# Kernel tuning notes

Hardware: AMD Instinct MI355X
Metric: run time of the kernel (lower is better)

## Reference

```python
import jax, jax.numpy as jnp
import numpy as np

N = 4096      # nodes
E = 131072    # edges (avg degree 32)
C = 256       # in/hidden channels
NC = 10       # classes
RATIO = 0.5
DEPTH = 2


def _build_adj(edge_index, w, n):
    # COO -> dense, duplicate edges summed (matches CSR coalescing)
    A = jnp.zeros((n, n), jnp.float32)
    return A.at[edge_index[0], edge_index[1]].add(w)


def _gcn(x, A, W, b, fill=2.0):
    # gcn_norm with improved=True: add_remaining_self_loops(fill=2.0),
    # deg from target (col) sums, sym norm; out[i] = sum_j Anorm[j,i] * (xW)[j]
    n = A.shape[0]
    idx = jnp.arange(n)
    diag = A[idx, idx]
    A = A.at[idx, idx].set(jnp.where(diag != 0, diag, fill))
    deg = A.sum(axis=0)
    dinv = jnp.where(deg > 0, jax.lax.rsqrt(deg), 0.0)
    An = dinv[:, None] * A * dinv[None, :]
    return An.T @ (x @ W) + b


def _augment(A):
    # remove_self_loops + add_self_loops(weight 1) == set diag to 1,
    # then adj @ adj, then remove self loops again
    n = A.shape[0]
    idx = jnp.arange(n)
    A = A.at[idx, idx].set(1.0)
    A2 = A @ A
    return A2.at[idx, idx].set(0.0)


def _pool(x, A, p, k):
    # TopKPooling: score = tanh(x.p / ||p||), keep top-k nodes, gate x by score
    score = jnp.tanh((x @ p) / jnp.linalg.norm(p))
    vals, perm = jax.lax.top_k(score, k)
    x2 = x[perm] * vals[:, None]
    A2 = A[perm][:, perm]   # filter_adj: keep edges with both ends selected
    return x2, A2


def reference(x, edge_index, w0, b0, w1, b1, w2, b2, p1, p2, wc, bc):
    A = _build_adj(edge_index, jnp.ones((edge_index.shape[1],), x.dtype), x.shape[0])
    x = jax.nn.relu(_gcn(x, A, w0, b0))
    k = x.shape[0]
    for (W, b, p) in ((w1, b1, p1), (w2, b2, p2)):
        A = _augment(A)
        k = int(np.ceil(RATIO * k))  # static per level (single graph)
        x, A = _pool(x, A, p, k)
        x = jax.nn.relu(_gcn(x, A, W, b))
    emb = x.mean(axis=0, keepdims=True)                      # global_mean_pool, batch all-zero
    emb = emb / jnp.maximum(jnp.linalg.norm(emb, axis=-1, keepdims=True), 1e-12)
    logits = emb @ wc.T + bc
    return emb, jax.nn.log_softmax(logits, axis=1)


def setup_inputs() -> dict:
    key = jax.random.key(0)
    ks = jax.random.split(key, 12)
    s = 1.0 / np.sqrt(C)
    return {
        'x': jax.random.normal(ks[0], (N, C), jnp.float32),
        'edge_index': jax.random.randint(ks[1], (2, E), 0, N, jnp.int64) if jax.config.jax_enable_x64 else jax.random.randint(ks[1], (2, E), 0, N, jnp.int32),
        'w0': jax.random.normal(ks[2], (C, C), jnp.float32) * s,
        'b0': jnp.zeros((C,), jnp.float32),
        'w1': jax.random.normal(ks[3], (C, C), jnp.float32) * s,
        'b1': jnp.zeros((C,), jnp.float32),
        'w2': jax.random.normal(ks[4], (C, C), jnp.float32) * s,
        'b2': jnp.zeros((C,), jnp.float32),
        'p1': jax.random.normal(ks[5], (C,), jnp.float32) * s,
        'p2': jax.random.normal(ks[6], (C,), jnp.float32) * s,
        'wc': jax.random.normal(ks[7], (NC, C), jnp.float32) * s,
        'bc': jnp.zeros((NC,), jnp.float32),
    }
```

## Files before the change

### kernel.cpp

```cpp
#include <hip/hip_runtime.h>
#include <math.h>

#define CH 256

typedef short short8 __attribute__((ext_vector_type(8)));
typedef float f32x4 __attribute__((ext_vector_type(4)));

__device__ inline ushort f2bf(float f) {
  unsigned u = __float_as_uint(f);
  unsigned r = (u + 0x7FFFu + ((u >> 16) & 1u)) >> 16;
  return (ushort)r;
}

__device__ inline void gload16(const void* g, void* l) {
  __builtin_amdgcn_global_load_lds((const __attribute__((address_space(1))) void*)g,
                                   (__attribute__((address_space(3))) void*)l, 16, 0, 0);
}


__global__ void scatter_edges(const int* __restrict__ ei, int E, int n, float* __restrict__ A) {
  int e = blockIdx.x * blockDim.x + threadIdx.x;
  if (e < E) atomicAdd(&A[(size_t)ei[e] * n + ei[E + e]], 1.0f);
}

template <int DIAGMODE>
__global__ __launch_bounds__(256) void transpose_deg(const float* __restrict__ In, int n,
                                                     ushort* __restrict__ O, float* __restrict__ deg,
                                                     int zn, size_t zoff) {
  __shared__ float t[64][65];
  int j0 = blockIdx.x * 64, i0 = blockIdx.y * 64;
  int tx = threadIdx.x & 63, ty4 = threadIdx.x >> 6;
  float s = 0.f;
#pragma unroll
  for (int r = 0; r < 64; r += 4) {
    int gi = i0 + ty4 + r, gj = j0 + tx;
    size_t idx = (size_t)gi * n + gj;
    float v = In[idx];
    for (int z = 1; z < zn; ++z) v += In[idx + (size_t)z * zoff];
    if (gi == gj) v = (DIAGMODE == 1) ? 2.0f : ((v != 0.f) ? v : 2.0f);
    t[ty4 + r][tx] = v;
    s += v;
  }
  atomicAdd(&deg[j0 + tx], s);
  __syncthreads();
#pragma unroll
  for (int r = 0; r < 64; r += 4) {
    int c = ty4 + r;
    O[(size_t)(j0 + c) * n + i0 + tx] = f2bf(t[tx][c]);
  }
}

__global__ __launch_bounds__(256) void topk_rank(const float* __restrict__ sc, int n, int k,
                                                 int* __restrict__ perm, float* __restrict__ vals) {
  extern __shared__ unsigned long long kbuf[];
  __shared__ int red[4][64];
  int tid = threadIdx.x;
  for (int i = tid; i < n; i += 256) {
    unsigned u = __float_as_uint(sc[i]);
    u = (u & 0x80000000u) ? ~u : (u | 0x80000000u);
    kbuf[i] = ((unsigned long long)u << 32) | (0xFFFFFFFFu - (unsigned)i);
  }
  __syncthreads();
  const int ti = tid & 63, tj = tid >> 6;
  const int i = blockIdx.x * 64 + ti;
  const unsigned long long ki = kbuf[i];
  int cnt = 0;
  const int q = n >> 2;
  const int jb = tj * q, je = jb + q;
#pragma unroll 4
  for (int j = jb; j < je; j += 2) {
    unsigned long long k0 = kbuf[j], k1 = kbuf[j + 1];
    cnt += (k0 > ki) + (k1 > ki);
  }
  red[tj][ti] = cnt;
  __syncthreads();
  if (tid < 64) {
    int r = red[0][ti] + red[1][ti] + red[2][ti] + red[3][ti];
    if (r < k) { perm[r] = i; vals[r] = sc[i]; }
  }
}

__global__ __launch_bounds__(256) void gather_fused(const float* __restrict__ Asrc, int zn, size_t zoff,
                                                    const ushort* __restrict__ At,
                                                    const int* __restrict__ perm, int n,
                                                    ushort* __restrict__ Arow, ushort* __restrict__ Brow,
                                                    const float* __restrict__ xin,
                                                    const float* __restrict__ vals, float* __restrict__ xo,
                                                    int nbcvt, int nbbf) {
  int bx = blockIdx.x;
  int m = blockIdx.y;
  int src = perm[m];
  if (bx < nbcvt) {
    int k4 = (bx * 256 + threadIdx.x) * 4;
    float4 v = *(const float4*)&Asrc[(size_t)src * n + k4];
    for (int z = 1; z < zn; ++z) {
      float4 u = *(const float4*)&Asrc[(size_t)z * zoff + (size_t)src * n + k4];
      v.x += u.x; v.y += u.y; v.z += u.z; v.w += u.w;
    }
    if (src >= k4 && src < k4 + 4) ((float*)&v)[src - k4] = 1.0f;
    ushort4 o;
    o.x = f2bf(v.x); o.y = f2bf(v.y); o.z = f2bf(v.z); o.w = f2bf(v.w);
    *(ushort4*)&Arow[(size_t)m * n + k4] = o;
  } else if (bx < nbcvt + nbbf) {
    int k8 = ((bx - nbcvt) * 256 + threadIdx.x) * 8;
    uint4 v = *(const uint4*)&At[(size_t)src * n + k8];
    if (src >= k8 && src < k8 + 8) ((ushort*)&v)[src - k8] = 0x3F80;
    *(uint4*)&Brow[(size_t)m * n + k8] = v;
  } else {
    xo[(size_t)m * CH + threadIdx.x] = xin[(size_t)src * CH + threadIdx.x] * vals[m];
  }
}


template <int BN>
__device__ inline void stage_tile(const ushort* ag, const ushort* bg, int ktOff,
                                  char* asb, char* bsb, int K) {
#pragma unroll
  for (int i = 0; i < 4; ++i)
    gload16(ag + (size_t)i * 32 * K + ktOff, asb + i * 4096);
#pragma unroll
  for (int i = 0; i < BN / 32; ++i)
    gload16(bg + (size_t)i * 32 * K + ktOff, bsb + i * 4096);
}

template <int BN>
__device__ inline void compute_tile(const ushort (*__restrict__ As)[64],
                                    const ushort (*__restrict__ Bs)[64],
                                    int wm, int wn, int lrow, int col0, int col1,
                                    f32x4 acc[4][BN / 32]) {
#pragma unroll
  for (int ks = 0; ks < 2; ++ks) {
    const int col = ks ? col1 : col0;
    short8 af[4], bf[BN / 32];
#pragma unroll
    for (int t = 0; t < 4; ++t)
      af[t] = *(const short8*)&As[wm + t * 16 + lrow][col];
#pragma unroll
    for (int t = 0; t < BN / 32; ++t)
      bf[t] = *(const short8*)&Bs[wn + t * 16 + lrow][col];
#pragma unroll
    for (int mt = 0; mt < 4; ++mt)
#pragma unroll
      for (int nt = 0; nt < BN / 32; ++nt)
        acc[mt][nt] = __builtin_amdgcn_mfma_f32_16x16x32_bf16(af[mt], bf[nt], acc[mt][nt], 0, 0, 0);
  }
}

template <int BN>
__global__ __launch_bounds__(256) void mfma_nt(const ushort* __restrict__ Aop,
                                               const ushort* __restrict__ Bop,
                                               float* __restrict__ C, int ldc,
                                               int K, int Ks, size_t zstride) {
  constexpr int NBUF = (BN == 128) ? 2 : 3;
  constexpr int NT = BN / 32;
  __shared__ ushort As[NBUF][128][64];
  __shared__ ushort Bs[NBUF][BN][64];
  const int tid = threadIdx.x;
  const int wave = tid >> 6, lane = tid & 63;
  const int wm = (wave & 1) * 64, wn = (wave >> 1) * (BN / 2);
  const int m0 = blockIdx.x * 128, n0 = blockIdx.y * BN;
  const int k0 = blockIdx.z * Ks;
  C += (size_t)blockIdx.z * zstride;
  const int lrow = lane & 15;
  const int q = lane >> 4;
  const int rx = lane & 7;
  const int col0 = ((q)     ^ rx) * 8;
  const int col1 = ((4 + q) ^ rx) * 8;
  const int srow = wave * 8 + (lane >> 3);
  const int scol = ((lane & 7) ^ (lane >> 3)) * 8;
  const ushort* ag = Aop + (size_t)(m0 + srow) * K + k0 + scol;
  const ushort* bg = Bop + (size_t)(n0 + srow) * K + k0 + scol;
  f32x4 acc[4][NT] = {};

  const int nk = Ks >> 6;

#define STAGE(bi, idx) stage_tile<BN>(ag, bg, (idx) * 64, \
    (char*)&As[bi][0][0] + wave * 1024, (char*)&Bs[bi][0][0] + wave * 1024, K)

  if constexpr (NBUF == 2) {
    STAGE(0, 0);
    if (1 < nk) STAGE(1, 1);
    int bi = 0;
    for (int t = 0; t < nk - 1; ++t) {
      asm volatile("s_waitcnt vmcnt(8)" ::: "memory");
      __builtin_amdgcn_s_barrier();
      __builtin_amdgcn_sched_barrier(0);
      compute_tile<BN>(As[bi], Bs[bi], wm, wn, lrow, col0, col1, acc);
      __builtin_amdgcn_sched_barrier(0);
      __builtin_amdgcn_s_barrier();
      if (t + 2 < nk) STAGE(bi, t + 2);
      bi ^= 1;
    }
    asm volatile("s_waitcnt vmcnt(0)" ::: "memory");
    __builtin_amdgcn_s_barrier();
    __builtin_amdgcn_sched_barrier(0);
    compute_tile<BN>(As[bi], Bs[bi], wm, wn, lrow, col0, col1, acc);
  } else {
    STAGE(0, 0);
    if (1 < nk) STAGE(1, 1);
    if (2 < nk) STAGE(2, 2);
    int bi = 0;
    for (int t = 0; t < nk - 2; ++t) {
      asm volatile("s_waitcnt vmcnt(12)" ::: "memory");
      __builtin_amdgcn_s_barrier();
      __builtin_amdgcn_sched_barrier(0);
      compute_tile<BN>(As[bi], Bs[bi], wm, wn, lrow, col0, col1, acc);
      __builtin_amdgcn_sched_barrier(0);
      __builtin_amdgcn_s_barrier();
      if (t + 3 < nk) STAGE(bi, t + 3);
      bi = (bi + 1 < 3) ? bi + 1 : 0;
    }
    asm volatile("s_waitcnt vmcnt(6)" ::: "memory");
    __builtin_amdgcn_s_barrier();
    __builtin_amdgcn_sched_barrier(0);
    compute_tile<BN>(As[bi], Bs[bi], wm, wn, lrow, col0, col1, acc);
    bi = (bi + 1 < 3) ? bi + 1 : 0;
    asm volatile("s_waitcnt vmcnt(0)" ::: "memory");
    __builtin_amdgcn_s_barrier();
    __builtin_amdgcn_sched_barrier(0);
    compute_tile<BN>(As[bi], Bs[bi], wm, wn, lrow, col0, col1, acc);
  }
#undef STAGE

  const int crow = (lane >> 4) * 4, ccol = lane & 15;
#pragma unroll
  for (int mt = 0; mt < 4; ++mt)
#pragma unroll
    for (int nt = 0; nt < NT; ++nt) {
      int gm = m0 + wm + mt * 16 + crow;
      int gn = n0 + wn + nt * 16 + ccol;
#pragma unroll
      for (int r = 0; r < 4; ++r)
        C[(size_t)(gm + r) * ldc + gn] = acc[mt][nt][r];
    }
}

__global__ void agg_epilogue(const float* __restrict__ Cred, size_t zstride, int zn,
                             float* __restrict__ deg,
                             const float* __restrict__ bias, float* __restrict__ xo,
                             const float* __restrict__ p, float* __restrict__ sc,
                             float* __restrict__ mclr) {
  int idx = blockIdx.x * 256 + threadIdx.x;
  int c4 = idx & 63;
  int m = idx >> 6;
  float d = deg[m];
  float s = (d > 0.f) ? 1.0f / sqrtf(d) : 0.f;
  if ((threadIdx.x & 63) == 0) deg[m] = 0.f;
  if (mclr && blockIdx.x == 0) mclr[threadIdx.x] = 0.f;
  float4 v = ((const float4*)Cred)[idx];
  for (int z = 1; z < zn; ++z) {
    float4 u = ((const float4*)(Cred + (size_t)z * zstride))[idx];
    v.x += u.x; v.y += u.y; v.z += u.z; v.w += u.w;
  }
  float4 b = ((const float4*)bias)[c4];
  v.x = fmaxf(fmaf(v.x, s, b.x), 0.f);
  v.y = fmaxf(fmaf(v.y, s, b.y), 0.f);
  v.z = fmaxf(fmaf(v.z, s, b.z), 0.f);
  v.w = fmaxf(fmaf(v.w, s, b.w), 0.f);
  ((float4*)xo)[idx] = v;
  if (p) {
    float4 pv = ((const float4*)p)[c4];
    float dot = v.x * pv.x + v.y * pv.y + v.z * pv.z + v.w * pv.w;
    float pn  = pv.x * pv.x + pv.y * pv.y + pv.z * pv.z + pv.w * pv.w;
    for (int off = 32; off; off >>= 1) {
      dot += __shfl_down(dot, off);
      pn  += __shfl_down(pn, off);
    }
    if ((threadIdx.x & 63) == 0) sc[m] = tanhf(dot / sqrtf(pn));
  }
}

__global__ __launch_bounds__(256) void xw_gemm(const float* __restrict__ Am,
                                               const float* __restrict__ Bm,
                                               ushort* __restrict__ Gt,
                                               int M, const float* __restrict__ deg) {
  __shared__ float As[16][64];
  __shared__ float Bs[16][64];
  const int tid = threadIdx.x;
  const int m0 = blockIdx.x * 64, n0 = blockIdx.y * 64;
  float acc[4][4] = {{0.f}};
  const int tm = tid & 15, tn = tid >> 4;

  for (int kt = 0; kt < CH; kt += 16) {
    __syncthreads();
    {
      int mm = tid >> 2, kq = (tid & 3) * 4;
      float4 v = *(const float4*)(Am + (size_t)(m0 + mm) * CH + kt + kq);
      As[kq + 0][mm] = v.x; As[kq + 1][mm] = v.y; As[kq + 2][mm] = v.z; As[kq + 3][mm] = v.w;
    }
#pragma unroll
    for (int r = 0; r < 4; ++r) {
      int idx = tid + r * 256;
      int kk = idx >> 6, nn = idx & 63;
      Bs[kk][nn] = Bm[(size_t)(kt + kk) * CH + (n0 + nn)];
    }
    __syncthreads();
#pragma unroll
    for (int kk = 0; kk < 16; ++kk) {
      float4 a = *(const float4*)&As[kk][tm * 4];
      float4 b = *(const float4*)&Bs[kk][tn * 4];
      acc[0][0] = fmaf(a.x, b.x, acc[0][0]);
      acc[0][1] = fmaf(a.x, b.y, acc[0][1]);
      acc[0][2] = fmaf(a.x, b.z, acc[0][2]);
      acc[0][3] = fmaf(a.x, b.w, acc[0][3]);
      acc[1][0] = fmaf(a.y, b.x, acc[1][0]);
      acc[1][1] = fmaf(a.y, b.y, acc[1][1]);
      acc[1][2] = fmaf(a.y, b.z, acc[1][2]);
      acc[1][3] = fmaf(a.y, b.w, acc[1][3]);
      acc[2][0] = fmaf(a.z, b.x, acc[2][0]);
      acc[2][1] = fmaf(a.z, b.y, acc[2][1]);
      acc[2][2] = fmaf(a.z, b.z, acc[2][2]);
      acc[2][3] = fmaf(a.z, b.w, acc[2][3]);
      acc[3][0] = fmaf(a.w, b.x, acc[3][0]);
      acc[3][1] = fmaf(a.w, b.y, acc[3][1]);
      acc[3][2] = fmaf(a.w, b.z, acc[3][2]);
      acc[3][3] = fmaf(a.w, b.w, acc[3][3]);
    }
  }

#pragma unroll
  for (int ii = 0; ii < 4; ++ii) {
    int m = m0 + tm * 4 + ii;
    float d = deg[m];
    float s = (d > 0.f) ? 1.0f / sqrtf(d) : 0.f;
#pragma unroll
    for (int jj = 0; jj < 4; ++jj) {
      int n = n0 + tn * 4 + jj;
      Gt[(size_t)n * M + m] = f2bf(s * acc[ii][jj]);
    }
  }
}


__global__ void mean_partial(const float* __restrict__ x2, float* __restrict__ macc) {
  int c = threadIdx.x;
  int j0 = blockIdx.x * 16;
  float s = 0.f;
#pragma unroll
  for (int j = 0; j < 16; ++j) s += x2[(size_t)(j0 + j) * CH + c];
  atomicAdd(&macc[c], s);
}

__global__ __launch_bounds__(256) void finalize2(const float* __restrict__ macc, int nr,
                                                 const float* __restrict__ wc,
                                                 const float* __restrict__ bc,
                                                 float* __restrict__ out) {
  __shared__ float semb[256];
  __shared__ float red[256];
  __shared__ float slog[16];
  int c = threadIdx.x;
  float emb = macc[c] / (float)nr;
  red[c] = emb * emb;
  __syncthreads();
  for (int off = 128; off; off >>= 1) {
    if (c < off) red[c] += red[c + off];
    __syncthreads();
  }
  float denom = fmaxf(sqrtf(red[0]), 1e-12f);
  float en = emb / denom;
  semb[c] = en;
  out[c] = en;
  __syncthreads();
  if (c < 10) {
    float l = bc[c];
    for (int t = 0; t < CH; ++t) l = fmaf(semb[t], wc[c * CH + t], l);
    slog[c] = l;
  }
  __syncthreads();
  if (c == 0) {
    float mx = slog[0];
    for (int j = 1; j < 10; ++j) mx = fmaxf(mx, slog[j]);
    float se = 0.f;
    for (int j = 0; j < 10; ++j) se += expf(slog[j] - mx);
    float lse = mx + logf(se);
    for (int j = 0; j < 10; ++j) out[CH + j] = slog[j] - lse;
  }
}


extern "C" void kernel_launch(void* const* d_in, const int* in_sizes, int n_in,
                              void* d_out, int out_size, void* d_ws, size_t ws_size,
                              hipStream_t stream) {
  const float* x  = (const float*)d_in[0];
  const int*   ei = (const int*)d_in[1];
  const float* w0 = (const float*)d_in[2];
  const float* b0 = (const float*)d_in[3];
  const float* w1 = (const float*)d_in[4];
  const float* b1 = (const float*)d_in[5];
  const float* w2 = (const float*)d_in[6];
  const float* b2 = (const float*)d_in[7];
  const float* p1 = (const float*)d_in[8];
  const float* p2 = (const float*)d_in[9];
  const float* wc = (const float*)d_in[10];
  const float* bc = (const float*)d_in[11];
  float* out = (float*)d_out;
  const int N0 = 4096, K1 = 2048, K2 = 1024;
  int E = in_sizes[1] / 2;

  float* W = (float*)d_ws;
  size_t off = 0;
  float* A    = W + off; off += (size_t)N0 * N0;
  float* deg  = W + off;
  off += (size_t)K1 * K1;
  ushort* At  = (ushort*)(W + off); off += (size_t)N0 * N0 / 2;
  ushort* Arow = (ushort*)(W + off); off += (size_t)K1 * N0 / 2;
  ushort* Brow = (ushort*)A;
  float* Paux = A + (size_t)8 * 1024 * 1024;
  float* Cred = (float*)Arow;
  float* x0   = W + off; off += (size_t)N0 * CH;
  ushort* Gt  = (ushort*)(W + off); off += (size_t)N0 * CH / 2;
  float* xp  = W + off; off += (size_t)K1 * CH;
  float* x1  = W + off; off += (size_t)K1 * CH;
  float* x2  = W + off; off += (size_t)K2 * CH;
  float* sc  = W + off; off += 4096;
  float* vals = W + off; off += 4096;
  float* macc = W + off; off += 256;
  int* perm1 = (int*)(W + off); off += 4096;
  int* perm2 = (int*)(W + off); off += 4096;

  hipMemsetAsync(A, 0, ((size_t)N0 * N0 + 4096) * 4, stream);
  scatter_edges<<<(E + 255) / 256, 256, 0, stream>>>(ei, E, N0, A);

  transpose_deg<0><<<dim3(N0 / 64, N0 / 64), 256, 0, stream>>>(A, N0, At, deg, 1, 0);
  xw_gemm<<<dim3(N0 / 64, CH / 64), 256, 0, stream>>>(x, w0, Gt, N0, deg);
  mfma_nt<64><<<dim3(N0 / 128, CH / 64, 4), 256, 0, stream>>>(At, Gt, Cred, CH, N0, N0 / 4, (size_t)N0 * CH);
  agg_epilogue<<<N0 / 4, 256, 0, stream>>>(Cred, (size_t)N0 * CH, 4, deg, b0, x0, p1, sc, nullptr);

  topk_rank<<<N0 / 64, 256, N0 * 8, stream>>>(sc, N0, K1, perm1, vals);

  gather_fused<<<dim3(N0 / 1024 + N0 / 2048 + 1, K1), 256, 0, stream>>>(
      A, 1, 0, At, perm1, N0, Arow, Brow, x0, vals, xp, N0 / 1024, N0 / 2048);
  mfma_nt<128><<<dim3(K1 / 128, K1 / 128, 2), 256, 0, stream>>>(Arow, Brow, Paux, K1, N0, N0 / 2, (size_t)K1 * K1);

  transpose_deg<1><<<dim3(K1 / 64, K1 / 64), 256, 0, stream>>>(Paux, K1, At, deg, 2, (size_t)K1 * K1);
  xw_gemm<<<dim3(K1 / 64, CH / 64), 256, 0, stream>>>(xp, w1, Gt, K1, deg);
  mfma_nt<64><<<dim3(K1 / 128, CH / 64, 8), 256, 0, stream>>>(At, Gt, Cred, CH, K1, K1 / 8, (size_t)K1 * CH);
  agg_epilogue<<<K1 / 4, 256, 0, stream>>>(Cred, (size_t)K1 * CH, 8, deg, b1, x1, p2, sc, nullptr);

  topk_rank<<<K1 / 64, 256, K1 * 8, stream>>>(sc, K1, K2, perm2, vals);

  gather_fused<<<dim3(K1 / 1024 + K1 / 2048 + 1, K2), 256, 0, stream>>>(
      Paux, 2, (size_t)K1 * K1, At, perm2, K1, Arow, Brow, x1, vals, xp, K1 / 1024, K1 / 2048);
  mfma_nt<128><<<dim3(K2 / 128, K2 / 128, 8), 256, 0, stream>>>(Arow, Brow, Paux, K2, K1, K1 / 8, (size_t)K2 * K2);

  transpose_deg<1><<<dim3(K2 / 64, K2 / 64), 256, 0, stream>>>(Paux, K2, At, deg, 8, (size_t)K2 * K2);
  xw_gemm<<<dim3(K2 / 64, CH / 64), 256, 0, stream>>>(xp, w2, Gt, K2, deg);
  mfma_nt<64><<<dim3(K2 / 128, CH / 64, 8), 256, 0, stream>>>(At, Gt, Cred, CH, K2, K2 / 8, (size_t)K2 * CH);
  agg_epilogue<<<K2 / 4, 256, 0, stream>>>(Cred, (size_t)K2 * CH, 8, deg, b2, x2, nullptr, nullptr, macc);

  mean_partial<<<K2 / 16, 256, 0, stream>>>(x2, macc);
  finalize2<<<1, 256, 0, stream>>>(macc, K2, wc, bc, out);
}
```

Before: 380.9 us.

## Fuse split-K reduction epilogue into GEMM via last-block counter

```diff
diff --git a/kernel.cpp b/kernel.cpp
--- a/kernel.cpp
+++ b/kernel.cpp
@@ -150,7 +150,10 @@
 __global__ __launch_bounds__(256) void mfma_nt(const ushort* __restrict__ Aop,
                                                const ushort* __restrict__ Bop,
                                                float* __restrict__ C, int ldc,
-                                               int K, int Ks, size_t zstride) {
+                                               int K, int Ks, size_t zstride,
+                                               int zn, unsigned* cnt, float* deg,
+                                               const float* bias, float* xo,
+                                               const float* pvec, float* sc, float* macc) {
   constexpr int NBUF = (BN == 128) ? 2 : 3;
   constexpr int NT = BN / 32;
   __shared__ ushort As[NBUF][128][64];
@@ -160,6 +163,7 @@
   const int wm = (wave & 1) * 64, wn = (wave >> 1) * (BN / 2);
   const int m0 = blockIdx.x * 128, n0 = blockIdx.y * BN;
   const int k0 = blockIdx.z * Ks;
+  float* Cbase = C;
   C += (size_t)blockIdx.z * zstride;
   const int lrow = lane & 15;
   const int q = lane >> 4;
@@ -233,40 +237,60 @@
       for (int r = 0; r < 4; ++r)
         C[(size_t)(gm + r) * ldc + gn] = acc[mt][nt][r];
     }
-}
-
-__global__ void agg_epilogue(const float* __restrict__ Cred, size_t zstride, int zn,
-                             float* __restrict__ deg,
-                             const float* __restrict__ bias, float* __restrict__ xo,
-                             const float* __restrict__ p, float* __restrict__ sc,
-                             float* __restrict__ mclr) {
-  int idx = blockIdx.x * 256 + threadIdx.x;
-  int c4 = idx & 63;
-  int m = idx >> 6;
-  float d = deg[m];
-  float s = (d > 0.f) ? 1.0f / sqrtf(d) : 0.f;
-  if ((threadIdx.x & 63) == 0) deg[m] = 0.f;
-  if (mclr && blockIdx.x == 0) mclr[threadIdx.x] = 0.f;
-  float4 v = ((const float4*)Cred)[idx];
-  for (int z = 1; z < zn; ++z) {
-    float4 u = ((const float4*)(Cred + (size_t)z * zstride))[idx];
-    v.x += u.x; v.y += u.y; v.z += u.z; v.w += u.w;
-  }
-  float4 b = ((const float4*)bias)[c4];
-  v.x = fmaxf(fmaf(v.x, s, b.x), 0.f);
-  v.y = fmaxf(fmaf(v.y, s, b.y), 0.f);
-  v.z = fmaxf(fmaf(v.z, s, b.z), 0.f);
-  v.w = fmaxf(fmaf(v.w, s, b.w), 0.f);
-  ((float4*)xo)[idx] = v;
-  if (p) {
-    float4 pv = ((const float4*)p)[c4];
-    float dot = v.x * pv.x + v.y * pv.y + v.z * pv.z + v.w * pv.w;
-    float pn  = pv.x * pv.x + pv.y * pv.y + pv.z * pv.z + pv.w * pv.w;
-    for (int off = 32; off; off >>= 1) {
-      dot += __shfl_down(dot, off);
-      pn  += __shfl_down(pn, off);
-    }
-    if ((threadIdx.x & 63) == 0) sc[m] = tanhf(dot / sqrtf(pn));
+
+  if (cnt) {
+    __threadfence();
+    __shared__ unsigned done;
+    if (tid == 0) done = atomicAdd(&cnt[blockIdx.x], 1u);
+    __syncthreads();
+    if (done == gridDim.y * gridDim.z - 1) {
+      __threadfence();
+      const int w = tid >> 6, c4 = tid & 63;
+      float4 msum = {0.f, 0.f, 0.f, 0.f};
+      const float4 b = ((const float4*)bias)[c4];
+      float4 pv;
+      float pn = 0.f;
+      if (pvec) {
+        pv = ((const float4*)pvec)[c4];
+        pn = pv.x * pv.x + pv.y * pv.y + pv.z * pv.z + pv.w * pv.w;
+        for (int off2 = 32; off2; off2 >>= 1) pn += __shfl_down(pn, off2);
+        pn = __shfl(pn, 0);
+      }
+      for (int r = 0; r < 32; ++r) {
+        const int m = m0 + r * 4 + w;
+        float d = deg[m];
+        float s = (d > 0.f) ? 1.0f / sqrtf(d) : 0.f;
+        float4 v = *(const float4*)&Cbase[(size_t)m * ldc + c4 * 4];
+        for (int z = 1; z < zn; ++z) {
+          float4 u = *(const float4*)&Cbase[(size_t)z * zstride + (size_t)m * ldc + c4 * 4];
+          v.x += u.x; v.y += u.y; v.z += u.z; v.w += u.w;
+        }
+        v.x = fmaxf(fmaf(v.x, s, b.x), 0.f);
+        v.y = fmaxf(fmaf(v.y, s, b.y), 0.f);
+        v.z = fmaxf(fmaf(v.z, s, b.z), 0.f);
+        v.w = fmaxf(fmaf(v.w, s, b.w), 0.f);
+        if (xo) ((float4*)xo)[(size_t)m * 64 + c4] = v;
+        if (c4 == 0) deg[m] = 0.f;
+        if (pvec) {
+          float dot = v.x * pv.x + v.y * pv.y + v.z * pv.z + v.w * pv.w;
+          for (int off2 = 32; off2; off2 >>= 1) dot += __shfl_down(dot, off2);
+          if (c4 == 0) sc[m] = tanhf(dot / sqrtf(pn));
+        }
+        if (macc) { msum.x += v.x; msum.y += v.y; msum.z += v.z; msum.w += v.w; }
+      }
+      if (macc) {
+        __shared__ float4 ssum[4][64];
+        ssum[w][c4] = msum;
+        __syncthreads();
+        if (w == 0) {
+          float4 t0 = ssum[0][c4], t1 = ssum[1][c4], t2 = ssum[2][c4], t3 = ssum[3][c4];
+          atomicAdd(&macc[c4 * 4 + 0], t0.x + t1.x + t2.x + t3.x);
+          atomicAdd(&macc[c4 * 4 + 1], t0.y + t1.y + t2.y + t3.y);
+          atomicAdd(&macc[c4 * 4 + 2], t0.z + t1.z + t2.z + t3.z);
+          atomicAdd(&macc[c4 * 4 + 3], t0.w + t1.w + t2.w + t3.w);
+        }
+      }
+    }
   }
 }
 
@@ -332,15 +356,6 @@
 }
 
 
-__global__ void mean_partial(const float* __restrict__ x2, float* __restrict__ macc) {
-  int c = threadIdx.x;
-  int j0 = blockIdx.x * 16;
-  float s = 0.f;
-#pragma unroll
-  for (int j = 0; j < 16; ++j) s += x2[(size_t)(j0 + j) * CH + c];
-  atomicAdd(&macc[c], s);
-}
-
 __global__ __launch_bounds__(256) void finalize2(const float* __restrict__ macc, int nr,
                                                  const float* __restrict__ wc,
                                                  const float* __restrict__ bc,
@@ -401,6 +416,10 @@
   size_t off = 0;
   float* A    = W + off; off += (size_t)N0 * N0;
   float* deg  = W + off;
+  unsigned* cnt0 = (unsigned*)(deg + 4096);
+  unsigned* cnt1 = cnt0 + 32;
+  unsigned* cnt2 = cnt1 + 16;
+  float* macc = (float*)(cnt0 + 64);
   off += (size_t)K1 * K1;
   ushort* At  = (ushort*)(W + off); off += (size_t)N0 * N0 / 2;
   ushort* Arow = (ushort*)(W + off); off += (size_t)K1 * N0 / 2;
@@ -411,43 +430,47 @@
   ushort* Gt  = (ushort*)(W + off); off += (size_t)N0 * CH / 2;
   float* xp  = W + off; off += (size_t)K1 * CH;
   float* x1  = W + off; off += (size_t)K1 * CH;
-  float* x2  = W + off; off += (size_t)K2 * CH;
   float* sc  = W + off; off += 4096;
   float* vals = W + off; off += 4096;
-  float* macc = W + off; off += 256;
   int* perm1 = (int*)(W + off); off += 4096;
   int* perm2 = (int*)(W + off); off += 4096;
 
-  hipMemsetAsync(A, 0, ((size_t)N0 * N0 + 4096) * 4, stream);
+  hipMemsetAsync(A, 0, ((size_t)N0 * N0 + 4096 + 64 + 256) * 4, stream);
   scatter_edges<<<(E + 255) / 256, 256, 0, stream>>>(ei, E, N0, A);
 
   transpose_deg<0><<<dim3(N0 / 64, N0 / 64), 256, 0, stream>>>(A, N0, At, deg, 1, 0);
   xw_gemm<<<dim3(N0 / 64, CH / 64), 256, 0, stream>>>(x, w0, Gt, N0, deg);
-  mfma_nt<64><<<dim3(N0 / 128, CH / 64, 4), 256, 0, stream>>>(At, Gt, Cred, CH, N0, N0 / 4, (size_t)N0 * CH);
-  agg_epilogue<<<N0 / 4, 256, 0, stream>>>(Cred, (size_t)N0 * CH, 4, deg, b0, x0, p1, sc, nullptr);
+  mfma_nt<64><<<dim3(N0 / 128, CH / 64, 4), 256, 0, stream>>>(
+      At, Gt, Cred, CH, N0, N0 / 4, (size_t)N0 * CH,
+      4, cnt0, deg, b0, x0, p1, sc, nullptr);
 
   topk_rank<<<N0 / 64, 256, N0 * 8, stream>>>(sc, N0, K1, perm1, vals);
 
   gather_fused<<<dim3(N0 / 1024 + N0 / 2048 + 1, K1), 256, 0, stream>>>(
       A, 1, 0, At, perm1, N0, Arow, Brow, x0, vals, xp, N0 / 1024, N0 / 2048);
-  mfma_nt<128><<<dim3(K1 / 128, K1 / 128, 2), 256, 0, stream>>>(Arow, Brow, Paux, K1, N0, N0 / 2, (size_t)K1 * K1);
+  mfma_nt<128><<<dim3(K1 / 128, K1 / 128, 2), 256, 0, stream>>>(
+      Arow, Brow, Paux, K1, N0, N0 / 2, (size_t)K1 * K1,
+      0, nullptr, nullptr, nullptr, nullptr, nullptr, nullptr, nullptr);
 
   transpose_deg<1><<<dim3(K1 / 64, K1 / 64), 256, 0, stream>>>(Paux, K1, At, deg, 2, (size_t)K1 * K1);
   xw_gemm<<<dim3(K1 / 64, CH / 64), 256, 0, stream>>>(xp, w1, Gt, K1, deg);
-  mfma_nt<64><<<dim3(K1 / 128, CH / 64, 8), 256, 0, stream>>>(At, Gt, Cred, CH, K1, K1 / 8, (size_t)K1 * CH);
-  agg_epilogue<<<K1 / 4, 256, 0, stream>>>(Cred, (size_t)K1 * CH, 8, deg, b1, x1, p2, sc, nullptr);
+  mfma_nt<64><<<dim3(K1 / 128, CH / 64, 8), 256, 0, stream>>>(
+      At, Gt, Cred, CH, K1, K1 / 8, (size_t)K1 * CH,
+      8, cnt1, deg, b1, x1, p2, sc, nullptr);
 
   topk_rank<<<K1 / 64, 256, K1 * 8, stream>>>(sc, K1, K2, perm2, vals);
 
   gather_fused<<<dim3(K1 / 1024 + K1 / 2048 + 1, K2), 256, 0, stream>>>(
       Paux, 2, (size_t)K1 * K1, At, perm2, K1, Arow, Brow, x1, vals, xp, K1 / 1024, K1 / 2048);
-  mfma_nt<128><<<dim3(K2 / 128, K2 / 128, 8), 256, 0, stream>>>(Arow, Brow, Paux, K2, K1, K1 / 8, (size_t)K2 * K2);
+  mfma_nt<128><<<dim3(K2 / 128, K2 / 128, 8), 256, 0, stream>>>(
+      Arow, Brow, Paux, K2, K1, K1 / 8, (size_t)K2 * K2,
+      0, nullptr, nullptr, nullptr, nullptr, nullptr, nullptr, nullptr);
 
   transpose_deg<1><<<dim3(K2 / 64, K2 / 64), 256, 0, stream>>>(Paux, K2, At, deg, 8, (size_t)K2 * K2);
   xw_gemm<<<dim3(K2 / 64, CH / 64), 256, 0, stream>>>(xp, w2, Gt, K2, deg);
-  mfma_nt<64><<<dim3(K2 / 128, CH / 64, 8), 256, 0, stream>>>(At, Gt, Cred, CH, K2, K2 / 8, (size_t)K2 * CH);
-  agg_epilogue<<<K2 / 4, 256, 0, stream>>>(Cred, (size_t)K2 * CH, 8, deg, b2, x2, nullptr, nullptr, macc);
-
-  mean_partial<<<K2 / 16, 256, 0, stream>>>(x2, macc);
+  mfma_nt<64><<<dim3(K2 / 128, CH / 64, 8), 256, 0, stream>>>(
+      At, Gt, Cred, CH, K2, K2 / 8, (size_t)K2 * CH,
+      8, cnt2, deg, b2, nullptr, nullptr, nullptr, macc);
+
   finalize2<<<1, 256, 0, stream>>>(macc, K2, wc, bc, out);
 }
```

Result: slower. 715.2 us (+87.8%).
